# Performance work log

Hardware: AMD Instinct MI355X
Metric: run time of the kernel (lower is better)

## Reference

```python
import jax, jax.numpy as jnp
import numpy as np

B, M, D, K = 64, 2_000_000, 32, 10
EPS = 1e-5            # kernel epsilon in _inverse_kernel
DENOM_C = 1e-5        # denominator_constant in _episodic_reward


def setup_inputs() -> dict:
    key = jax.random.key(0)
    kq, km = jax.random.split(key)
    query = jax.random.normal(kq, (B, D), dtype=jnp.float32)
    memory = jax.random.normal(km, (M, D), dtype=jnp.float32)
    return {"query": query, "memory": memory, "k": K}


def reference(query, memory, k):
    # Squared Euclidean distances [B, M] via the expanded form (no [B,M,D] intermediate).
    q2 = jnp.sum(query * query, axis=-1, keepdims=True)          # [B, 1]
    m2 = jnp.sum(memory * memory, axis=-1)                       # [M]
    sq = jnp.maximum(q2 + m2[None, :] - 2.0 * (query @ memory.T), 0.0)  # [B, M]
    # Running mean of squared distances (vectorized fixed point of RunningMean;
    # stateful numpy update in the original -> no gradient through it).
    mean_sq = jax.lax.stop_gradient(jnp.mean(sq))
    # _inverse_kernel: eps / (d^2 / mean + eps)
    kdist = EPS / (sq / mean_sq + EPS)                           # [B, M]
    # sklearn kneighbors picks the k SMALLEST metric values.
    neg_topk, _ = jax.lax.top_k(-kdist, k)                       # [B, k]
    neighbor_sum = -jnp.sum(neg_topk, axis=-1)                   # [B]
    # episodic reward: 1 / sqrt(sum(neighbor kernel distances) + c)
    return 1.0 / jnp.sqrt(neighbor_sum + DENOM_C)
```

## Files before the change

### kernel.cpp

```cpp
#include <hip/hip_runtime.h>
#include <hip/hip_bf16.h>
#include <float.h>
#include <math.h>

typedef short short8 __attribute__((ext_vector_type(8)));
typedef float f32x4  __attribute__((ext_vector_type(4)));

#define KEPS   1e-5f
#define DENOMC 1e-5f

__device__ __forceinline__ short f2bf(float x) {
    return __builtin_bit_cast(short, __float2bfloat16(x));
}

__device__ __forceinline__ void gload_lds16(const void* g, void* l) {
    __builtin_amdgcn_global_load_lds(
        (const __attribute__((address_space(1))) void*)g,
        (__attribute__((address_space(3))) void*)l,
        16, 0, 0);
}

__device__ __forceinline__ void top10_insert(float (&lst)[10], float s) {
    if (s > lst[0]) {
        lst[0] = s;
        #pragma unroll
        for (int i = 1; i < 10; ++i) {
            float lo = fminf(lst[0], lst[i]);
            float hi = fmaxf(lst[0], lst[i]);
            lst[0] = lo; lst[i] = hi;
        }
    }
}

__global__ __launch_bounds__(256, 8) void ep_main(
    const float* __restrict__ q, const float* __restrict__ mem,
    float* __restrict__ part_top,
    float* __restrict__ part_sums,
    int nb, int ntiles)
{
    __shared__ __align__(16) char smemc[17408];

    const int tid  = threadIdx.x;
    const int lane = tid & 63;
    const int wave = tid >> 6;
    const int g    = lane >> 4;
    const int c    = lane & 15;
    const int bid  = blockIdx.x;

    const int tpb = ntiles / nb;
    const int rem = ntiles % nb;
    const int t0  = bid * tpb + (bid < rem ? bid : rem);
    const int cnt = tpb + (bid < rem ? 1 : 0);

    short8 qfrag[4];
    #pragma unroll
    for (int h = 0; h < 4; ++h) {
        const float* qp = q + (h * 16 + c) * 32 + g * 8;
        f32x4 w0 = *(const f32x4*)qp;
        f32x4 w1 = *(const f32x4*)(qp + 4);
        short8 f;
        f[0]=f2bf(-2.f*w0[0]); f[1]=f2bf(-2.f*w0[1]); f[2]=f2bf(-2.f*w0[2]); f[3]=f2bf(-2.f*w0[3]);
        f[4]=f2bf(-2.f*w1[0]); f[5]=f2bf(-2.f*w1[1]); f[6]=f2bf(-2.f*w1[2]); f[7]=f2bf(-2.f*w1[3]);
        qfrag[h] = f;
    }

    float t1[16];
    #pragma unroll
    for (int i = 0; i < 16; ++i) t1[i] = -FLT_MAX;
    float cs[8];
    #pragma unroll
    for (int r = 0; r < 8; ++r) cs[r] = 0.f;
    float sumsq = 0.f;

    char* ring = smemc + wave * 4096;
    const int    sw    = ((lane >> 3) & 3) << 1;
    const size_t so    = (size_t)((lane ^ sw) * 16);
    const size_t rdoff = (size_t)(((c * 8 + g * 2) ^ ((c & 3) << 1)) * 16);

    auto process = [&](const char* buf) {
        const f32x4* rp = (const f32x4*)(buf + rdoff);
        f32x4 v0 = rp[0];
        f32x4 v1 = rp[1];

        float ps;
        ps = v0[0] * v0[0];
        ps = fmaf(v0[1], v0[1], ps);
        ps = fmaf(v0[2], v0[2], ps);
        ps = fmaf(v0[3], v0[3], ps);
        ps = fmaf(v1[0], v1[0], ps);
        ps = fmaf(v1[1], v1[1], ps);
        ps = fmaf(v1[2], v1[2], ps);
        ps = fmaf(v1[3], v1[3], ps);
        float m2 = ps + __shfl_xor(ps, 16, 64);
        m2 = m2 + __shfl_xor(m2, 32, 64);

        sumsq += ps;
        cs[0] += v0[0]; cs[1] += v0[1]; cs[2] += v0[2]; cs[3] += v0[3];
        cs[4] += v1[0]; cs[5] += v1[1]; cs[6] += v1[2]; cs[7] += v1[3];

        short8 mf;
        mf[0]=f2bf(v0[0]); mf[1]=f2bf(v0[1]); mf[2]=f2bf(v0[2]); mf[3]=f2bf(v0[3]);
        mf[4]=f2bf(v1[0]); mf[5]=f2bf(v1[1]); mf[6]=f2bf(v1[2]); mf[7]=f2bf(v1[3]);

        const f32x4 zero = {0.f, 0.f, 0.f, 0.f};
        #pragma unroll
        for (int h = 0; h < 4; ++h) {
            f32x4 acc = __builtin_amdgcn_mfma_f32_16x16x32_bf16(qfrag[h], mf, zero, 0, 0, 0);
            t1[h*4+0] = fmaxf(t1[h*4+0], acc[0] + m2);
            t1[h*4+1] = fmaxf(t1[h*4+1], acc[1] + m2);
            t1[h*4+2] = fmaxf(t1[h*4+2], acc[2] + m2);
            t1[h*4+3] = fmaxf(t1[h*4+3], acc[3] + m2);
        }
    };

    const char* gsrc = (const char*)mem + (size_t)t0 * 8192 + (size_t)wave * 2048 + so;

    gload_lds16(gsrc,        ring);
    gload_lds16(gsrc + 1024, ring + 1024);
    gsrc += 8192;

    for (int i = 0; i < cnt; ++i) {
        const bool more = (i + 1) < cnt;
        if (more) {
            char* dst = ring + ((i + 1) & 1) * 2048;
            gload_lds16(gsrc,        dst);
            gload_lds16(gsrc + 1024, dst + 1024);
            gsrc += 8192;
            asm volatile("s_waitcnt vmcnt(2)" ::: "memory");
        } else {
            asm volatile("s_waitcnt vmcnt(0)" ::: "memory");
        }
        process(ring + (i & 1) * 2048);
    }

    __syncthreads();
    float (*ltop)[65]  = (float (*)[65])smemc;
    float (*red)[4][8] = (float (*)[4][8])(smemc + 16640);
    float* ssred       = (float*)(smemc + 17152);

    const int col = wave * 16 + c;
    #pragma unroll
    for (int h = 0; h < 4; ++h) {
        #pragma unroll
        for (int r = 0; r < 4; ++r)
            ltop[h * 16 + g * 4 + r][col] = t1[h * 4 + r];
    }

    #pragma unroll
    for (int r = 0; r < 8; ++r) {
        float v = cs[r];
        v += __shfl_xor(v, 1, 64);
        v += __shfl_xor(v, 2, 64);
        v += __shfl_xor(v, 4, 64);
        v += __shfl_xor(v, 8, 64);
        cs[r] = v;
    }
    float ssv = sumsq;
    ssv += __shfl_xor(ssv, 1, 64);
    ssv += __shfl_xor(ssv, 2, 64);
    ssv += __shfl_xor(ssv, 4, 64);
    ssv += __shfl_xor(ssv, 8, 64);
    ssv += __shfl_xor(ssv, 16, 64);
    ssv += __shfl_xor(ssv, 32, 64);
    if (c == 0) {
        #pragma unroll
        for (int r = 0; r < 8; ++r) red[wave][g][r] = cs[r];
    }
    if (lane == 0) ssred[wave] = ssv;
    __syncthreads();

    if (tid < 32) {
        float a = red[0][tid >> 3][tid & 7] + red[1][tid >> 3][tid & 7]
                + red[2][tid >> 3][tid & 7] + red[3][tid >> 3][tid & 7];
        part_sums[(size_t)tid * nb + bid] = a;
    } else if (tid == 32) {
        part_sums[(size_t)32 * nb + bid] = ssred[0] + ssred[1] + ssred[2] + ssred[3];
    }

    if (tid < 64) {
        float lst[10];
        #pragma unroll
        for (int i = 0; i < 10; ++i) lst[i] = -FLT_MAX;
        #pragma unroll 4
        for (int s2 = 0; s2 < 64; ++s2) top10_insert(lst, ltop[tid][s2]);
        #pragma unroll
        for (int i = 0; i < 10; ++i)
            part_top[((size_t)tid * nb + bid) * 10 + i] = lst[i];
    }
}

__global__ __launch_bounds__(256) void ep_tail(
    const float* __restrict__ q, const float* __restrict__ part_top,
    const float* __restrict__ part_sums, float* __restrict__ out,
    int nb, int Mrows)
{
    const int b    = blockIdx.x;
    const int tid  = threadIdx.x;
    const int lane = tid & 63;
    const int wave = tid >> 6;

    __shared__ float smem[256 * 33];
    __shared__ float colsum_a[33];
    __shared__ float w4[4];
    __shared__ float mean_s, q2_s;

    if (tid < 64) {
        float x = (tid < 32) ? q[b * 32 + tid] : 0.f;
        float a = x * x;
        a += __shfl_xor(a, 1, 64);
        a += __shfl_xor(a, 2, 64);
        a += __shfl_xor(a, 4, 64);
        a += __shfl_xor(a, 8, 64);
        a += __shfl_xor(a, 16, 64);
        if (tid == 0) q2_s = a;
    }

    float a2 = 0.f;
    #pragma unroll
    for (int e = 0; e < 8; ++e) {
        float x = q[tid * 8 + e];
        a2 = fmaf(x, x, a2);
    }
    a2 += __shfl_xor(a2, 1, 64);
    a2 += __shfl_xor(a2, 2, 64);
    a2 += __shfl_xor(a2, 4, 64);
    a2 += __shfl_xor(a2, 8, 64);
    a2 += __shfl_xor(a2, 16, 64);
    a2 += __shfl_xor(a2, 32, 64);
    if (lane == 0) w4[wave] = a2;

    float acc[33];
    #pragma unroll
    for (int c2 = 0; c2 < 33; ++c2) acc[c2] = 0.f;
    for (int i = tid; i < nb; i += 256) {
        #pragma unroll
        for (int c2 = 0; c2 < 33; ++c2) acc[c2] += part_sums[(size_t)c2 * nb + i];
    }
    #pragma unroll
    for (int c2 = 0; c2 < 33; ++c2) smem[tid * 33 + c2] = acc[c2];
    __syncthreads();
    if (tid < 33) {
        float a = 0.f;
        #pragma unroll 16
        for (int j = 0; j < 256; ++j) a += smem[j * 33 + tid];
        colsum_a[tid] = a;
    }
    __syncthreads();

    if (tid < 32) {
        float qs = 0.f;
        #pragma unroll 8
        for (int bb = 0; bb < 64; ++bb) qs += q[bb * 32 + tid];
        float dq = qs * colsum_a[tid];
        dq += __shfl_xor(dq, 1, 64);
        dq += __shfl_xor(dq, 2, 64);
        dq += __shfl_xor(dq, 4, 64);
        dq += __shfl_xor(dq, 8, 64);
        dq += __shfl_xor(dq, 16, 64);
        if (tid == 0) {
            double q2sum = (double)w4[0] + (double)w4[1] + (double)w4[2] + (double)w4[3];
            double sumsq = (double)colsum_a[32];
            double Md    = (double)Mrows;
            mean_s = (float)((Md * q2sum + 64.0 * sumsq - 2.0 * (double)dq) / (64.0 * Md));
        }
    }
    __syncthreads();

    float lst[10];
    #pragma unroll
    for (int i = 0; i < 10; ++i) lst[i] = -FLT_MAX;
    const float* pt = part_top + (size_t)b * nb * 10;
    for (int i = tid; i < nb; i += 256) {
        const float* pp = pt + (size_t)i * 10;
        #pragma unroll
        for (int r = 0; r < 10; ++r) top10_insert(lst, pp[r]);
    }
    #pragma unroll
    for (int r = 0; r < 10; ++r) smem[tid * 10 + r] = lst[r];
    __syncthreads();

    if (tid < 32) {
        float m[10];
        #pragma unroll
        for (int i = 0; i < 10; ++i) m[i] = -FLT_MAX;
        for (int j2 = 0; j2 < 8; ++j2) {
            #pragma unroll
            for (int r = 0; r < 10; ++r) top10_insert(m, smem[(tid * 8 + j2) * 10 + r]);
        }
        #pragma unroll
        for (int r = 0; r < 10; ++r) smem[2560 + tid * 10 + r] = m[r];
    }
    __syncthreads();

    if (tid == 0) {
        float m[10];
        #pragma unroll
        for (int i = 0; i < 10; ++i) m[i] = -FLT_MAX;
        for (int j2 = 0; j2 < 32; ++j2) {
            #pragma unroll
            for (int r = 0; r < 10; ++r) top10_insert(m, smem[2560 + j2 * 10 + r]);
        }
        const float mean = mean_s;
        const float q2b  = q2_s;
        float sum = 0.f;
        #pragma unroll
        for (int r = 0; r < 10; ++r) {
            float sq = m[r] + q2b;
            sq = fmaxf(sq, 0.f);
            sum += KEPS / (sq / mean + KEPS);
        }
        out[b] = 1.0f / sqrtf(sum + DENOMC);
    }
}

extern "C" void kernel_launch(void* const* d_in, const int* in_sizes, int n_in,
                              void* d_out, int out_size, void* d_ws, size_t ws_size,
                              hipStream_t stream)
{
    const float* q   = (const float*)d_in[0];
    const float* mem = (const float*)d_in[1];
    float* out = (float*)d_out;

    const int Mrows  = in_sizes[1] / 32;
    const int ntiles = Mrows / 64;

    int nb = 2048;
    while (nb > 64 && ((size_t)nb * 673 + 64) * sizeof(float) > ws_size) nb >>= 1;
    if (nb > ntiles) nb = ntiles;

    float* part_top  = (float*)d_ws;
    float* part_sums = part_top + (size_t)64 * nb * 10;

    ep_main<<<dim3(nb), dim3(256), 0, stream>>>(q, mem, part_top, part_sums, nb, ntiles);
    ep_tail<<<dim3(64), dim3(256), 0, stream>>>(q, part_top, part_sums, out, nb, Mrows);
}
```

Measured before the change: 101.8 us.

## Replace LDS-staged global loads with direct register double-buffered loads

The memory tile streaming drops the global_load_lds ring buffer and reads each lane's memory rows straight into registers, processing four tiles per batch with ping-pong register buffers for prefetch. It also halves the number of blocks and lowers the occupancy hint in launch bounds so the kernel has room for the extra live registers. This removes LDS round trips and the s_waitcnt-based staging, at the cost of higher register pressure and less latency hiding from occupancy. Per-lane reads are 32 contiguous bytes at a 128-byte stride, which may coalesce less well than the swizzled LDS path did.

```diff
diff --git a/kernel.cpp b/kernel.cpp
--- a/kernel.cpp
+++ b/kernel.cpp
@@ -13,13 +13,6 @@
     return __builtin_bit_cast(short, __float2bfloat16(x));
 }
 
-__device__ __forceinline__ void gload_lds16(const void* g, void* l) {
-    __builtin_amdgcn_global_load_lds(
-        (const __attribute__((address_space(1))) void*)g,
-        (__attribute__((address_space(3))) void*)l,
-        16, 0, 0);
-}
-
 __device__ __forceinline__ void top10_insert(float (&lst)[10], float s) {
     if (s > lst[0]) {
         lst[0] = s;
@@ -32,13 +25,15 @@
     }
 }
 
-__global__ __launch_bounds__(256, 8) void ep_main(
+__global__ __launch_bounds__(256, 4) void ep_main(
     const float* __restrict__ q, const float* __restrict__ mem,
     float* __restrict__ part_top,
     float* __restrict__ part_sums,
     int nb, int ntiles)
 {
-    __shared__ __align__(16) char smemc[17408];
+    __shared__ float smem[4224];
+    __shared__ float red[4][4][8];
+    __shared__ float ssred[4];
 
     const int tid  = threadIdx.x;
     const int lane = tid & 63;
@@ -72,16 +67,10 @@
     for (int r = 0; r < 8; ++r) cs[r] = 0.f;
     float sumsq = 0.f;
 
-    char* ring = smemc + wave * 4096;
-    const int    sw    = ((lane >> 3) & 3) << 1;
-    const size_t so    = (size_t)((lane ^ sw) * 16);
-    const size_t rdoff = (size_t)(((c * 8 + g * 2) ^ ((c & 3) << 1)) * 16);
-
-    auto process = [&](const char* buf) {
-        const f32x4* rp = (const f32x4*)(buf + rdoff);
-        f32x4 v0 = rp[0];
-        f32x4 v1 = rp[1];
-
+    const char* pbase = (const char*)mem + (size_t)t0 * 8192
+                      + (size_t)wave * 2048 + (size_t)(c * 128 + g * 32);
+
+    auto process = [&](f32x4 v0, f32x4 v1) {
         float ps;
         ps = v0[0] * v0[0];
         ps = fmaf(v0[1], v0[1], ps);
@@ -113,30 +102,48 @@
         }
     };
 
-    const char* gsrc = (const char*)mem + (size_t)t0 * 8192 + (size_t)wave * 2048 + so;
-
-    gload_lds16(gsrc,        ring);
-    gload_lds16(gsrc + 1024, ring + 1024);
-    gsrc += 8192;
-
-    for (int i = 0; i < cnt; ++i) {
-        const bool more = (i + 1) < cnt;
-        if (more) {
-            char* dst = ring + ((i + 1) & 1) * 2048;
-            gload_lds16(gsrc,        dst);
-            gload_lds16(gsrc + 1024, dst + 1024);
-            gsrc += 8192;
-            asm volatile("s_waitcnt vmcnt(2)" ::: "memory");
-        } else {
-            asm volatile("s_waitcnt vmcnt(0)" ::: "memory");
-        }
-        process(ring + (i & 1) * 2048);
-    }
-
-    __syncthreads();
-    float (*ltop)[65]  = (float (*)[65])smemc;
-    float (*red)[4][8] = (float (*)[4][8])(smemc + 16640);
-    float* ssred       = (float*)(smemc + 17152);
+    f32x4 a0,a1,a2,a3,a4,a5,a6,a7;
+    f32x4 b0,b1,b2,b3,b4,b5,b6,b7;
+
+    #define LOADX(r0,r1,r2,r3,r4,r5,r6,r7, P) do {                         \
+        const char* _p = (P);                                              \
+        r0 = *(const f32x4*)(_p);          r1 = *(const f32x4*)(_p + 16);  \
+        r2 = *(const f32x4*)(_p + 8192);   r3 = *(const f32x4*)(_p + 8208);\
+        r4 = *(const f32x4*)(_p + 16384);  r5 = *(const f32x4*)(_p + 16400);\
+        r6 = *(const f32x4*)(_p + 24576);  r7 = *(const f32x4*)(_p + 24592);\
+    } while (0)
+    #define PROCX(r0,r1,r2,r3,r4,r5,r6,r7) do {                            \
+        process(r0, r1); process(r2, r3); process(r4, r5); process(r6, r7);\
+    } while (0)
+
+    const int nb4  = cnt >> 2;
+    const int cnt4 = nb4 << 2;
+
+    if (nb4 > 0) {
+        LOADX(a0,a1,a2,a3,a4,a5,a6,a7, pbase);
+        #pragma unroll 1
+        for (int b = 0; b < nb4; ++b) {
+            if ((b & 1) == 0) {
+                if (b + 1 < nb4) LOADX(b0,b1,b2,b3,b4,b5,b6,b7, pbase + (size_t)(b+1) * 32768);
+                PROCX(a0,a1,a2,a3,a4,a5,a6,a7);
+            } else {
+                if (b + 1 < nb4) LOADX(a0,a1,a2,a3,a4,a5,a6,a7, pbase + (size_t)(b+1) * 32768);
+                PROCX(b0,b1,b2,b3,b4,b5,b6,b7);
+            }
+        }
+    }
+    #pragma unroll 1
+    for (int t = cnt4; t < cnt; ++t) {
+        const char* p = pbase + (size_t)t * 8192;
+        f32x4 v0 = *(const f32x4*)(p);
+        f32x4 v1 = *(const f32x4*)(p + 16);
+        process(v0, v1);
+    }
+    #undef LOADX
+    #undef PROCX
+
+    __syncthreads();
+    float (*ltop)[65] = (float (*)[65])smem;
 
     const int col = wave * 16 + c;
     #pragma unroll
@@ -324,7 +331,7 @@
     const int Mrows  = in_sizes[1] / 32;
     const int ntiles = Mrows / 64;
 
-    int nb = 2048;
+    int nb = 1024;
     while (nb > 64 && ((size_t)nb * 673 + 64) * sizeof(float) > ws_size) nb >>= 1;
     if (nb > ntiles) nb = ntiles;
 
```

Result: slower. 191.1 us (+87.8%).
